# Kernel tuning notes

Hardware: AMD Instinct MI355X
Metric: run time of the kernel (lower is better)

## Reference

```python
import jax, jax.numpy as jnp
import numpy as np

KERNEL_EPSILON = 0.001


def setup_inputs() -> dict:
    key = jax.random.key(0)
    k1, k2, k3 = jax.random.split(key, 3)
    B, H, S, D = 4, 16, 4096, 64
    return {
        "query": jax.random.normal(k1, (B, H, S, D), dtype=jnp.float32),
        "key": jax.random.normal(k2, (B, H, S, D), dtype=jnp.float32),
        "value": jax.random.normal(k3, (B, H, S, D), dtype=jnp.float32),
        "mask": jnp.ones((B, S), dtype=jnp.float32),
    }


def reference(query, key, value, mask):
    # ReLU feature map + epsilon
    q = jax.nn.relu(query) + KERNEL_EPSILON          # [B,H,S,D]
    k = jax.nn.relu(key) + KERNEL_EPSILON            # [B,H,S,D]
    k = k * mask[:, None, :, None]                   # mask keys
    # kv: [B,H,D,E] = sum_s k[...,s,d] * v[...,s,e]  (done first: linear attention)
    kv = jnp.einsum("bhsd,bhse->bhde", k, value)
    numerator = jnp.einsum("bhsd,bhde->bhse", q, kv)  # [B,H,S,D]
    k_sum = jnp.sum(k, axis=-2)                       # [B,H,D]
    denominator = jnp.einsum("bhsd,bhd->bhs", q, k_sum)[..., None]
    return numerator / denominator
```

## Files before the change

### kernel.cpp

```cpp
#include <hip/hip_runtime.h>


namespace {
constexpr int kB = 4, kH = 16, kS = 4096, kD = 64;
constexpr int kBH = kB * kH;
constexpr float kEps = 0.001f;

constexpr int CH1 = 8;
constexpr int CS1 = kS / CH1;
constexpr int TS  = 16;
constexpr int CH2 = 16;
constexpr int CS2 = kS / CH2;

constexpr int KVSZ = kD * kD;
constexpr int SEG  = KVSZ + kD;
}

__global__ __launch_bounds__(256)
void pa_kv_partial(const float* __restrict__ key, const float* __restrict__ value,
                   const float* __restrict__ mask, float* __restrict__ P) {
  const int bh    = blockIdx.x / CH1;
  const int chunk = blockIdx.x - bh * CH1;
  const int b     = bh / kH;
  const int s0    = chunk * CS1;
  const float* kbase = key   + (size_t)bh * kS * kD;
  const float* vbase = value + (size_t)bh * kS * kD;
  const float* mbase = mask  + (size_t)b * kS;

  __shared__ float ks[TS][kD];
  __shared__ float vs[TS][kD];

  const int tid  = threadIdx.x;
  const int ti   = tid >> 4;
  const int tj   = tid & 15;
  const int lcol = tj << 2;

  float acc[4][4];
#pragma unroll
  for (int r = 0; r < 4; ++r)
#pragma unroll
    for (int c = 0; c < 4; ++c) acc[r][c] = 0.f;
  float ksx = 0.f, ksy = 0.f, ksz = 0.f, ksw = 0.f;

  float4 kq = *(const float4*)(kbase + ((size_t)(s0 + ti)) * kD + lcol);
  float4 vq = *(const float4*)(vbase + ((size_t)(s0 + ti)) * kD + lcol);
  float  m  = mbase[s0 + ti];

  for (int t = 0; t < CS1; t += TS) {
    float4 kt;
    kt.x = (fmaxf(kq.x, 0.f) + kEps) * m;
    kt.y = (fmaxf(kq.y, 0.f) + kEps) * m;
    kt.z = (fmaxf(kq.z, 0.f) + kEps) * m;
    kt.w = (fmaxf(kq.w, 0.f) + kEps) * m;
    float4 vt = vq;

    __syncthreads();
    *(float4*)&ks[ti][lcol] = kt;
    *(float4*)&vs[ti][lcol] = vt;
    ksx += kt.x; ksy += kt.y; ksz += kt.z; ksw += kt.w;
    __syncthreads();

    if (t + TS < CS1) {
      const int sn = s0 + t + TS + ti;
      kq = *(const float4*)(kbase + (size_t)sn * kD + lcol);
      vq = *(const float4*)(vbase + (size_t)sn * kD + lcol);
      m  = mbase[sn];
    }

#pragma unroll
    for (int ss = 0; ss < TS; ++ss) {
      const float4 kf = *(const float4*)&ks[ss][ti << 2];
      const float4 vf = *(const float4*)&vs[ss][tj << 2];
      acc[0][0] = fmaf(kf.x, vf.x, acc[0][0]);
      acc[0][1] = fmaf(kf.x, vf.y, acc[0][1]);
      acc[0][2] = fmaf(kf.x, vf.z, acc[0][2]);
      acc[0][3] = fmaf(kf.x, vf.w, acc[0][3]);
      acc[1][0] = fmaf(kf.y, vf.x, acc[1][0]);
      acc[1][1] = fmaf(kf.y, vf.y, acc[1][1]);
      acc[1][2] = fmaf(kf.y, vf.z, acc[1][2]);
      acc[1][3] = fmaf(kf.y, vf.w, acc[1][3]);
      acc[2][0] = fmaf(kf.z, vf.x, acc[2][0]);
      acc[2][1] = fmaf(kf.z, vf.y, acc[2][1]);
      acc[2][2] = fmaf(kf.z, vf.z, acc[2][2]);
      acc[2][3] = fmaf(kf.z, vf.w, acc[2][3]);
      acc[3][0] = fmaf(kf.w, vf.x, acc[3][0]);
      acc[3][1] = fmaf(kf.w, vf.y, acc[3][1]);
      acc[3][2] = fmaf(kf.w, vf.z, acc[3][2]);
      acc[3][3] = fmaf(kf.w, vf.w, acc[3][3]);
    }
  }

  float* Pd = P + ((size_t)bh * CH1 + chunk) * SEG;
#pragma unroll
  for (int r = 0; r < 4; ++r) {
    float4 o = make_float4(acc[r][0], acc[r][1], acc[r][2], acc[r][3]);
    *(float4*)&Pd[(size_t)(4 * ti + r) * kD + 4 * tj] = o;
  }

  __syncthreads();
  ks[ti][lcol + 0] = ksx;
  ks[ti][lcol + 1] = ksy;
  ks[ti][lcol + 2] = ksz;
  ks[ti][lcol + 3] = ksw;
  __syncthreads();
  if (tid < kD) {
    float tot = 0.f;
#pragma unroll
    for (int r = 0; r < TS; ++r) tot += ks[r][tid];
    Pd[KVSZ + tid] = tot;
  }
}

__global__ __launch_bounds__(256)
void pa_reduce(const float* __restrict__ P, float* __restrict__ R) {
  const int gid = blockIdx.x * 256 + threadIdx.x;
  const int o = gid * 4;
  if (o >= kBH * SEG) return;
  const int bh  = o / SEG;
  const int pos = o - bh * SEG;
  const float* base = P + (size_t)bh * CH1 * SEG + pos;
  float ax = 0.f, ay = 0.f, az = 0.f, aw = 0.f;
#pragma unroll
  for (int c = 0; c < CH1; ++c) {
    const float4 t = *(const float4*)(base + (size_t)c * SEG);
    ax += t.x; ay += t.y; az += t.z; aw += t.w;
  }
  *(float4*)&R[o] = make_float4(ax, ay, az, aw);
}

__global__ __launch_bounds__(256)
void pa_out(const float* __restrict__ query, const float* __restrict__ R,
            float* __restrict__ out) {
  const int bh    = blockIdx.x / CH2;
  const int chunk = blockIdx.x - bh * CH2;
  const int s     = chunk * CS2 + threadIdx.x;

  __shared__ float kvs[KVSZ];
  __shared__ float ksums[kD];

  const float* Rb = R + (size_t)bh * SEG;
#pragma unroll
  for (int it = 0; it < 4; ++it) {
    const int idx = (threadIdx.x + it * 256) * 4;
    *(float4*)&kvs[idx] = *(const float4*)&Rb[idx];
  }
  if (threadIdx.x < kD) ksums[threadIdx.x] = Rb[KVSZ + threadIdx.x];
  __syncthreads();

  const float* qrow = query + ((size_t)bh * kS + s) * kD;
  float q[kD];
#pragma unroll
  for (int d4 = 0; d4 < kD / 4; ++d4) {
    const float4 t = *(const float4*)(qrow + d4 * 4);
    q[d4 * 4 + 0] = fmaxf(t.x, 0.f) + kEps;
    q[d4 * 4 + 1] = fmaxf(t.y, 0.f) + kEps;
    q[d4 * 4 + 2] = fmaxf(t.z, 0.f) + kEps;
    q[d4 * 4 + 3] = fmaxf(t.w, 0.f) + kEps;
  }

  float den = 0.f;
#pragma unroll
  for (int d = 0; d < kD; ++d) den = fmaf(q[d], ksums[d], den);
  const float invden = 1.0f / den;

  float* orow = out + ((size_t)bh * kS + s) * kD;
  for (int e4 = 0; e4 < kD / 4; ++e4) {
    float ax = 0.f, ay = 0.f, az = 0.f, aw = 0.f;
#pragma unroll
    for (int d = 0; d < kD; ++d) {
      const float4 kvv = *(const float4*)&kvs[d * kD + e4 * 4];
      ax = fmaf(q[d], kvv.x, ax);
      ay = fmaf(q[d], kvv.y, ay);
      az = fmaf(q[d], kvv.z, az);
      aw = fmaf(q[d], kvv.w, aw);
    }
    *(float4*)&orow[e4 * 4] = make_float4(ax * invden, ay * invden, az * invden, aw * invden);
  }
}

extern "C" void kernel_launch(void* const* d_in, const int* in_sizes, int n_in,
                              void* d_out, int out_size, void* d_ws, size_t ws_size,
                              hipStream_t stream) {
  const float* query = (const float*)d_in[0];
  const float* key   = (const float*)d_in[1];
  const float* value = (const float*)d_in[2];
  const float* mask  = (const float*)d_in[3];
  float* outp = (float*)d_out;

  float* P = (float*)d_ws;
  float* R = P + (size_t)kBH * CH1 * SEG;

  hipLaunchKernelGGL(pa_kv_partial, dim3(kBH * CH1), dim3(256), 0, stream,
                     key, value, mask, P);
  hipLaunchKernelGGL(pa_reduce, dim3((kBH * SEG / 4 + 255) / 256), dim3(256), 0, stream,
                     P, R);
  hipLaunchKernelGGL(pa_out, dim3(kBH * CH2), dim3(256), 0, stream,
                     query, R, outp);
}
```

Baseline: 267.0 us.

## Rewrite linear attention kernels with per-wave 8x8 KV tiles and staged output

Restructures the KV partial kernel so that each 64-lane wave owns its own shared-memory tile and accumulates an 8x8 register tile per lane, which removes block-wide barriers. Each wave writes its own partial, and the workspace size decides how many chunks are used. The reduce kernel permutes the partial layout back to row-major. The output kernel now reads KV straight from global memory (uniform, cache-resident) instead of shared memory and stages results through padded shared memory for coalesced row stores. The aim is to raise FMA-per-load reuse and cut synchronisation, at the cost of more registers and larger partial buffers.

After: 255.7 us. 4.2% less time.

```diff
diff --git a/kernel.cpp b/kernel.cpp
--- a/kernel.cpp
+++ b/kernel.cpp
@@ -6,175 +6,204 @@
 constexpr int kBH = kB * kH;
 constexpr float kEps = 0.001f;
 
-constexpr int CH1 = 8;
-constexpr int CS1 = kS / CH1;
-constexpr int TS  = 16;
-constexpr int CH2 = 16;
-constexpr int CS2 = kS / CH2;
-
 constexpr int KVSZ = kD * kD;
 constexpr int SEG  = KVSZ + kD;
+constexpr int F4PS = SEG / 4;
+}
+
+__global__ __launch_bounds__(256, 2)
+void pa_kv_partial(const float* __restrict__ key, const float* __restrict__ value,
+                   const float* __restrict__ mask, float* __restrict__ P, int ch1) {
+  __shared__ float smem[4096];
+
+  const int tid  = threadIdx.x;
+  const int wid  = tid >> 6;
+  const int lane = tid & 63;
+
+  const int bh    = blockIdx.x / ch1;
+  const int chunk = blockIdx.x - bh * ch1;
+  const int b     = bh >> 4;
+  const int rows  = kS / ch1;
+  const int s0    = chunk * rows;
+  const int tiles = rows >> 5;
+
+  const float* kb = key   + (size_t)bh * kS * kD;
+  const float* vb = value + (size_t)bh * kS * kD;
+  const float* mb = mask  + (size_t)b * kS;
+
+  float* ksT = smem + wid * 1024;
+  float* vsT = smem + wid * 1024 + 512;
+
+  const int lrow = lane >> 4;
+  const int lcol = (lane & 15) << 2;
+  const int ti   = lane >> 3;
+  const int tj   = lane & 7;
+
+  float acc[8][8];
+#pragma unroll
+  for (int i = 0; i < 8; ++i)
+#pragma unroll
+    for (int j = 0; j < 8; ++j) acc[i][j] = 0.f;
+  float4 ksacc = make_float4(0.f, 0.f, 0.f, 0.f);
+
+  int ts = s0 + wid * 8;
+  float4 kq0 = *(const float4*)(kb + (size_t)(ts + lrow) * kD + lcol);
+  float4 kq1 = *(const float4*)(kb + (size_t)(ts + 4 + lrow) * kD + lcol);
+  float4 vq0 = *(const float4*)(vb + (size_t)(ts + lrow) * kD + lcol);
+  float4 vq1 = *(const float4*)(vb + (size_t)(ts + 4 + lrow) * kD + lcol);
+  float  m0  = mb[ts + lrow];
+  float  m1  = mb[ts + 4 + lrow];
+
+  for (int t = 0; t < tiles; ++t) {
+    float4 kt0, kt1;
+    kt0.x = (fmaxf(kq0.x, 0.f) + kEps) * m0;
+    kt0.y = (fmaxf(kq0.y, 0.f) + kEps) * m0;
+    kt0.z = (fmaxf(kq0.z, 0.f) + kEps) * m0;
+    kt0.w = (fmaxf(kq0.w, 0.f) + kEps) * m0;
+    kt1.x = (fmaxf(kq1.x, 0.f) + kEps) * m1;
+    kt1.y = (fmaxf(kq1.y, 0.f) + kEps) * m1;
+    kt1.z = (fmaxf(kq1.z, 0.f) + kEps) * m1;
+    kt1.w = (fmaxf(kq1.w, 0.f) + kEps) * m1;
+
+    ksacc.x += kt0.x + kt1.x;
+    ksacc.y += kt0.y + kt1.y;
+    ksacc.z += kt0.z + kt1.z;
+    ksacc.w += kt0.w + kt1.w;
+
+    *(float4*)&ksT[lrow * 64 + lcol]       = kt0;
+    *(float4*)&ksT[(lrow + 4) * 64 + lcol] = kt1;
+    *(float4*)&vsT[lrow * 64 + lcol]       = vq0;
+    *(float4*)&vsT[(lrow + 4) * 64 + lcol] = vq1;
+
+    if (t + 1 < tiles) {
+      ts += 32;
+      kq0 = *(const float4*)(kb + (size_t)(ts + lrow) * kD + lcol);
+      kq1 = *(const float4*)(kb + (size_t)(ts + 4 + lrow) * kD + lcol);
+      vq0 = *(const float4*)(vb + (size_t)(ts + lrow) * kD + lcol);
+      vq1 = *(const float4*)(vb + (size_t)(ts + 4 + lrow) * kD + lcol);
+      m0  = mb[ts + lrow];
+      m1  = mb[ts + 4 + lrow];
+    }
+
+#pragma unroll
+    for (int ss = 0; ss < 8; ++ss) {
+      const float4 kf0 = *(const float4*)&ksT[ss * 64 + 8 * ti];
+      const float4 kf1 = *(const float4*)&ksT[ss * 64 + 8 * ti + 4];
+      const float4 vf0 = *(const float4*)&vsT[ss * 64 + 8 * tj];
+      const float4 vf1 = *(const float4*)&vsT[ss * 64 + 8 * tj + 4];
+      const float ka[8] = {kf0.x, kf0.y, kf0.z, kf0.w, kf1.x, kf1.y, kf1.z, kf1.w};
+      const float va[8] = {vf0.x, vf0.y, vf0.z, vf0.w, vf1.x, vf1.y, vf1.z, vf1.w};
+#pragma unroll
+      for (int i = 0; i < 8; ++i)
+#pragma unroll
+        for (int j = 0; j < 8; ++j) acc[i][j] = fmaf(ka[i], va[j], acc[i][j]);
+    }
+  }
+
+  float* Pd = P + (size_t)(blockIdx.x * 4 + wid) * SEG;
+#pragma unroll
+  for (int i = 0; i < 8; ++i)
+#pragma unroll
+    for (int jj = 0; jj < 2; ++jj) {
+      const int j = i * 2 + jj;
+      const float4 o = make_float4(acc[i][jj * 4 + 0], acc[i][jj * 4 + 1],
+                                   acc[i][jj * 4 + 2], acc[i][jj * 4 + 3]);
+      *(float4*)&Pd[(size_t)(j * 64 + lane) * 4] = o;
+    }
+
+  ksacc.x += __shfl_xor(ksacc.x, 16); ksacc.x += __shfl_xor(ksacc.x, 32);
+  ksacc.y += __shfl_xor(ksacc.y, 16); ksacc.y += __shfl_xor(ksacc.y, 32);
+  ksacc.z += __shfl_xor(ksacc.z, 16); ksacc.z += __shfl_xor(ksacc.z, 32);
+  ksacc.w += __shfl_xor(ksacc.w, 16); ksacc.w += __shfl_xor(ksacc.w, 32);
+  if (lane < 16) *(float4*)&Pd[KVSZ + 4 * lane] = ksacc;
 }
 
 __global__ __launch_bounds__(256)
-void pa_kv_partial(const float* __restrict__ key, const float* __restrict__ value,
-                   const float* __restrict__ mask, float* __restrict__ P) {
-  const int bh    = blockIdx.x / CH1;
-  const int chunk = blockIdx.x - bh * CH1;
-  const int b     = bh / kH;
-  const int s0    = chunk * CS1;
-  const float* kbase = key   + (size_t)bh * kS * kD;
-  const float* vbase = value + (size_t)bh * kS * kD;
-  const float* mbase = mask  + (size_t)b * kS;
-
-  __shared__ float ks[TS][kD];
-  __shared__ float vs[TS][kD];
-
-  const int tid  = threadIdx.x;
-  const int ti   = tid >> 4;
-  const int tj   = tid & 15;
-  const int lcol = tj << 2;
-
-  float acc[4][4];
-#pragma unroll
-  for (int r = 0; r < 4; ++r)
-#pragma unroll
-    for (int c = 0; c < 4; ++c) acc[r][c] = 0.f;
-  float ksx = 0.f, ksy = 0.f, ksz = 0.f, ksw = 0.f;
-
-  float4 kq = *(const float4*)(kbase + ((size_t)(s0 + ti)) * kD + lcol);
-  float4 vq = *(const float4*)(vbase + ((size_t)(s0 + ti)) * kD + lcol);
-  float  m  = mbase[s0 + ti];
-
-  for (int t = 0; t < CS1; t += TS) {
-    float4 kt;
-    kt.x = (fmaxf(kq.x, 0.f) + kEps) * m;
-    kt.y = (fmaxf(kq.y, 0.f) + kEps) * m;
-    kt.z = (fmaxf(kq.z, 0.f) + kEps) * m;
-    kt.w = (fmaxf(kq.w, 0.f) + kEps) * m;
-    float4 vt = vq;
-
-    __syncthreads();
-    *(float4*)&ks[ti][lcol] = kt;
-    *(float4*)&vs[ti][lcol] = vt;
-    ksx += kt.x; ksy += kt.y; ksz += kt.z; ksw += kt.w;
-    __syncthreads();
-
-    if (t + TS < CS1) {
-      const int sn = s0 + t + TS + ti;
-      kq = *(const float4*)(kbase + (size_t)sn * kD + lcol);
-      vq = *(const float4*)(vbase + (size_t)sn * kD + lcol);
-      m  = mbase[sn];
-    }
-
-#pragma unroll
-    for (int ss = 0; ss < TS; ++ss) {
-      const float4 kf = *(const float4*)&ks[ss][ti << 2];
-      const float4 vf = *(const float4*)&vs[ss][tj << 2];
-      acc[0][0] = fmaf(kf.x, vf.x, acc[0][0]);
-      acc[0][1] = fmaf(kf.x, vf.y, acc[0][1]);
-      acc[0][2] = fmaf(kf.x, vf.z, acc[0][2]);
-      acc[0][3] = fmaf(kf.x, vf.w, acc[0][3]);
-      acc[1][0] = fmaf(kf.y, vf.x, acc[1][0]);
-      acc[1][1] = fmaf(kf.y, vf.y, acc[1][1]);
-      acc[1][2] = fmaf(kf.y, vf.z, acc[1][2]);
-      acc[1][3] = fmaf(kf.y, vf.w, acc[1][3]);
-      acc[2][0] = fmaf(kf.z, vf.x, acc[2][0]);
-      acc[2][1] = fmaf(kf.z, vf.y, acc[2][1]);
-      acc[2][2] = fmaf(kf.z, vf.z, acc[2][2]);
-      acc[2][3] = fmaf(kf.z, vf.w, acc[2][3]);
-      acc[3][0] = fmaf(kf.w, vf.x, acc[3][0]);
-      acc[3][1] = fmaf(kf.w, vf.y, acc[3][1]);
-      acc[3][2] = fmaf(kf.w, vf.z, acc[3][2]);
-      acc[3][3] = fmaf(kf.w, vf.w, acc[3][3]);
-    }
-  }
-
-  float* Pd = P + ((size_t)bh * CH1 + chunk) * SEG;
-#pragma unroll
-  for (int r = 0; r < 4; ++r) {
-    float4 o = make_float4(acc[r][0], acc[r][1], acc[r][2], acc[r][3]);
-    *(float4*)&Pd[(size_t)(4 * ti + r) * kD + 4 * tj] = o;
-  }
-
-  __syncthreads();
-  ks[ti][lcol + 0] = ksx;
-  ks[ti][lcol + 1] = ksy;
-  ks[ti][lcol + 2] = ksz;
-  ks[ti][lcol + 3] = ksw;
-  __syncthreads();
-  if (tid < kD) {
-    float tot = 0.f;
-#pragma unroll
-    for (int r = 0; r < TS; ++r) tot += ks[r][tid];
-    Pd[KVSZ + tid] = tot;
-  }
-}
-
-__global__ __launch_bounds__(256)
-void pa_reduce(const float* __restrict__ P, float* __restrict__ R) {
+void pa_reduce(const float* __restrict__ P, float* __restrict__ R, int nseg) {
   const int gid = blockIdx.x * 256 + threadIdx.x;
-  const int o = gid * 4;
-  if (o >= kBH * SEG) return;
-  const int bh  = o / SEG;
-  const int pos = o - bh * SEG;
-  const float* base = P + (size_t)bh * CH1 * SEG + pos;
+  if (gid >= kBH * F4PS) return;
+  const int bh  = gid / F4PS;
+  const int pos = gid - bh * F4PS;
+
+  const float* base = P + (size_t)bh * nseg * SEG + (size_t)pos * 4;
   float ax = 0.f, ay = 0.f, az = 0.f, aw = 0.f;
-#pragma unroll
-  for (int c = 0; c < CH1; ++c) {
+  for (int c = 0; c < nseg; ++c) {
     const float4 t = *(const float4*)(base + (size_t)c * SEG);
     ax += t.x; ay += t.y; az += t.z; aw += t.w;
   }
-  *(float4*)&R[o] = make_float4(ax, ay, az, aw);
+
+  int dpos;
+  if (pos < KVSZ / 4) {
+    const int j  = pos >> 6, ln = pos & 63;
+    const int d  = 8 * (ln >> 3) + (j >> 1);
+    const int e4 = 2 * (ln & 7) + (j & 1);
+    dpos = d * 16 + e4;
+  } else {
+    dpos = pos;
+  }
+  *(float4*)&R[(size_t)bh * SEG + (size_t)dpos * 4] = make_float4(ax, ay, az, aw);
 }
 
 __global__ __launch_bounds__(256)
 void pa_out(const float* __restrict__ query, const float* __restrict__ R,
             float* __restrict__ out) {
-  const int bh    = blockIdx.x / CH2;
-  const int chunk = blockIdx.x - bh * CH2;
-  const int s     = chunk * CS2 + threadIdx.x;
-
-  __shared__ float kvs[KVSZ];
-  __shared__ float ksums[kD];
-
-  const float* Rb = R + (size_t)bh * SEG;
-#pragma unroll
-  for (int it = 0; it < 4; ++it) {
-    const int idx = (threadIdx.x + it * 256) * 4;
-    *(float4*)&kvs[idx] = *(const float4*)&Rb[idx];
-  }
-  if (threadIdx.x < kD) ksums[threadIdx.x] = Rb[KVSZ + threadIdx.x];
-  __syncthreads();
+  __shared__ float ost[64 * 68];
+
+  const int tid    = threadIdx.x;
+  const int bh     = blockIdx.x >> 4;
+  const int rowblk = blockIdx.x & 15;
+  const int s      = rowblk * 256 + tid;
 
   const float* qrow = query + ((size_t)bh * kS + s) * kD;
-  float q[kD];
-#pragma unroll
-  for (int d4 = 0; d4 < kD / 4; ++d4) {
-    const float4 t = *(const float4*)(qrow + d4 * 4);
-    q[d4 * 4 + 0] = fmaxf(t.x, 0.f) + kEps;
-    q[d4 * 4 + 1] = fmaxf(t.y, 0.f) + kEps;
-    q[d4 * 4 + 2] = fmaxf(t.z, 0.f) + kEps;
-    q[d4 * 4 + 3] = fmaxf(t.w, 0.f) + kEps;
-  }
-
+  const float* Rb   = R + (size_t)bh * SEG;
+
+  float4 acc[16];
+#pragma unroll
+  for (int e = 0; e < 16; ++e) acc[e] = make_float4(0.f, 0.f, 0.f, 0.f);
   float den = 0.f;
-#pragma unroll
-  for (int d = 0; d < kD; ++d) den = fmaf(q[d], ksums[d], den);
-  const float invden = 1.0f / den;
-
-  float* orow = out + ((size_t)bh * kS + s) * kD;
-  for (int e4 = 0; e4 < kD / 4; ++e4) {
-    float ax = 0.f, ay = 0.f, az = 0.f, aw = 0.f;
-#pragma unroll
-    for (int d = 0; d < kD; ++d) {
-      const float4 kvv = *(const float4*)&kvs[d * kD + e4 * 4];
-      ax = fmaf(q[d], kvv.x, ax);
-      ay = fmaf(q[d], kvv.y, ay);
-      az = fmaf(q[d], kvv.z, az);
-      aw = fmaf(q[d], kvv.w, aw);
-    }
-    *(float4*)&orow[e4 * 4] = make_float4(ax * invden, ay * invden, az * invden, aw * invden);
+
+#pragma unroll 4
+  for (int d4 = 0; d4 < 16; ++d4) {
+    const float4 qv = *(const float4*)(qrow + 4 * d4);
+    const float qd[4] = {fmaxf(qv.x, 0.f) + kEps, fmaxf(qv.y, 0.f) + kEps,
+                         fmaxf(qv.z, 0.f) + kEps, fmaxf(qv.w, 0.f) + kEps};
+#pragma unroll
+    for (int dd = 0; dd < 4; ++dd) {
+      const int d = 4 * d4 + dd;
+      den = fmaf(qd[dd], Rb[KVSZ + d], den);
+      const float* kvr = Rb + d * 64;
+#pragma unroll
+      for (int e = 0; e < 16; ++e) {
+        acc[e].x = fmaf(qd[dd], kvr[4 * e + 0], acc[e].x);
+        acc[e].y = fmaf(qd[dd], kvr[4 * e + 1], acc[e].y);
+        acc[e].z = fmaf(qd[dd], kvr[4 * e + 2], acc[e].z);
+        acc[e].w = fmaf(qd[dd], kvr[4 * e + 3], acc[e].w);
+      }
+    }
+  }
+
+  const float inv = 1.0f / den;
+#pragma unroll
+  for (int e = 0; e < 16; ++e) {
+    acc[e].x *= inv; acc[e].y *= inv; acc[e].z *= inv; acc[e].w *= inv;
+  }
+
+  float* ob = out + ((size_t)bh * kS + (size_t)rowblk * 256) * kD;
+  const int wid = tid >> 6, l = tid & 63;
+  for (int bb = 0; bb < 4; ++bb) {
+    if (wid == bb) {
+#pragma unroll
+      for (int e = 0; e < 16; ++e) *(float4*)&ost[l * 68 + 4 * e] = acc[e];
+    }
+    __syncthreads();
+#pragma unroll
+    for (int jj = 0; jj < 4; ++jj) {
+      const int g = tid + 256 * jj;
+      const int r = g >> 4, c = g & 15;
+      *(float4*)&ob[(size_t)(bb * 64 + r) * kD + 4 * c] =
+          *(const float4*)&ost[r * 68 + 4 * c];
+    }
+    __syncthreads();
   }
 }
 
@@ -187,13 +216,20 @@
   const float* mask  = (const float*)d_in[3];
   float* outp = (float*)d_out;
 
+  auto need = [](int ch1) -> size_t {
+    return (size_t)(kBH * 4 * ch1 + kBH) * SEG * sizeof(float);
+  };
+  int CH1 = 2;
+  if (ws_size >= need(8)) CH1 = 8;
+  else if (ws_size >= need(4)) CH1 = 4;
+
   float* P = (float*)d_ws;
-  float* R = P + (size_t)kBH * CH1 * SEG;
+  float* R = P + (size_t)kBH * 4 * CH1 * SEG;
 
   hipLaunchKernelGGL(pa_kv_partial, dim3(kBH * CH1), dim3(256), 0, stream,
-                     key, value, mask, P);
-  hipLaunchKernelGGL(pa_reduce, dim3((kBH * SEG / 4 + 255) / 256), dim3(256), 0, stream,
-                     P, R);
-  hipLaunchKernelGGL(pa_out, dim3(kBH * CH2), dim3(256), 0, stream,
+                     key, value, mask, P, CH1);
+  hipLaunchKernelGGL(pa_reduce, dim3((kBH * F4PS + 255) / 256), dim3(256), 0, stream,
+                     P, R, 4 * CH1);
+  hipLaunchKernelGGL(pa_out, dim3(kBH * 16), dim3(256), 0, stream,
                      query, R, outp);
 }
```
